# Optimization experiments

Hardware: AMD Instinct MI355X
Metric: run time of the kernel (lower is better)

The kernel has to match this reference:

```python
import jax, jax.numpy as jnp
import numpy as np

L = 8          # fixed number of instance labels (0 = background), all assumed present
DV = 0.5       # delta_v
DD = 1.5       # delta_d
LOSS_WEIGHT = 1.0


def _safe_norm(x, axis):
    sq = jnp.sum(x * x, axis=axis)
    pos = sq > 0
    return jnp.sqrt(jnp.where(pos, sq, 1.0)) * pos.astype(x.dtype)


def _per_image(emb, inst, kern, tmask):
    # emb: [D,H,W], inst: [H,W] int, kern/tmask: [H,W] float
    D, H, W = emb.shape
    HW = H * W
    tm = (tmask > 0.5).astype(inst.dtype)
    kb = (kern > 0.5).astype(inst.dtype)
    inst = inst * tm
    inst_k = (inst * kb).reshape(-1)          # kernel-region labels
    inst_f = inst.reshape(-1)                 # full-region labels
    emb_f = emb.reshape(D, -1).T              # [HW, D]

    # --- generate_coef: first/second occurrence (row-major) of each label ---
    flat = jnp.arange(HW)
    eq = inst_f[None, :] == jnp.arange(L)[:, None]          # [L, HW]
    idxs = jnp.where(eq, flat[None, :], HW)
    first = jnp.min(idxs, axis=1)
    second = jnp.min(jnp.where(idxs == first[:, None], HW, idxs), axis=1)
    first = jnp.minimum(first, HW - 1)
    second = jnp.minimum(second, HW - 1)
    r0, c0 = first // W, first % W
    r1, c1 = second // W, second % W
    # pos_id = (tmp[0,0], tmp[1,0], tmp[0,-1], tmp[1,-1]) as in the source
    pos = jnp.stack([r0, r1, c0, c1], axis=1).astype(jnp.float32)  # [L,4]
    diag = jnp.sqrt(jnp.float32(H * H + W * W))
    coef_diag = jnp.exp(jnp.sqrt((pos[:, 0] - pos[:, 2]) ** 2 +
                                 (pos[:, 1] - pos[:, 3]) ** 2) / diag / 2.0)
    zmask = (jnp.arange(L) > 0).astype(jnp.float32)          # skip label 0
    coef_diag = coef_diag * zmask
    s = pos[:, 0] + pos[:, 2]
    t = pos[:, 1] + pos[:, 3]
    dp = jnp.sqrt((s[:, None] - s[None, :]) ** 2 + (t[:, None] - t[None, :]) ** 2)
    coef_off = 1.0 - 20.0 * jnp.exp(-4.0 - 2.5 * dp / diag)
    eye = jnp.eye(L, dtype=bool)
    coef = jnp.where(eye, coef_diag[:, None], coef_off)
    coef = coef * zmask[:, None] * zmask[None, :]

    # --- per-label kernel means (segment mean) ---
    ones = jnp.ones((HW,), jnp.float32)
    cnt_k = jax.ops.segment_sum(ones, inst_k, num_segments=L)
    mean = jax.ops.segment_sum(emb_f, inst_k, num_segments=L)
    mean = mean / jnp.maximum(cnt_k, 1.0)[:, None]           # [L, D]
    mean = mean * zmask[:, None]

    # --- l_agg: per-pixel distance to own-label mean, segment-mean per label ---
    mean_px = mean[inst_f]                                   # [HW, D] gather
    dist = _safe_norm(emb_f - mean_px, axis=1)
    cd_px = coef_diag[inst_f]
    val = jnp.log(jax.nn.relu(cd_px * dist - DV) ** 2 + 1.0)
    cnt = jax.ops.segment_sum(ones, inst_f, num_segments=L)
    l_agg_per = jax.ops.segment_sum(val, inst_f, num_segments=L) / jnp.maximum(cnt, 1.0)
    l_agg = jnp.mean(l_agg_per[1:])

    # --- l_dis: coefficient-weighted pairwise hinge between means ---
    Dn = _safe_norm(mean[:, None, :] - mean[None, :, :], axis=-1)  # [L, L]
    pm = (~eye) & (zmask[:, None] > 0) & (zmask[None, :] > 0)
    vals = jnp.log(jax.nn.relu(2.0 * DD - coef * Dn) ** 2 + 1.0)
    l_dis = jnp.sum(jnp.where(pm, vals, 0.0)) / ((L - 1) * (L - 2))

    # --- l_reg ---
    l_reg = jnp.mean(jnp.log(_safe_norm(mean, axis=1) + 1.0)) * 0.001
    return l_agg + l_dis + l_reg


def reference(emb, instance, kernel, training_mask, bboxes):
    # bboxes is accepted but unused, matching the original forward_single
    loss_batch = jax.vmap(_per_image)(emb, instance, kernel, training_mask)
    return LOSS_WEIGHT * jnp.mean(loss_batch)


def setup_inputs() -> dict:
    key = jax.random.key(0)
    k1, k2, k3, k4, k5 = jax.random.split(key, 5)
    B, D, H, W = 8, 4, 640, 640
    emb = jax.random.normal(k1, (B, D, H, W), dtype=jnp.float32)
    instance = jax.random.randint(k2, (B, H, W), 0, L, dtype=jnp.int32)
    kernel = jax.random.uniform(k3, (B, H, W), dtype=jnp.float32)
    training_mask = jax.random.uniform(k4, (B, H, W), dtype=jnp.float32)
    bboxes = jax.random.uniform(k5, (B, 10, 4), dtype=jnp.float32)
    return {"emb": emb, "instance": instance, "kernel": kernel,
            "training_mask": training_mask, "bboxes": bboxes}
```

## Files before the change

### kernel.cpp

```cpp
#include <hip/hip_runtime.h>

#define B_    8
#define D_    4
#define H_    640
#define W_    640
#define HW_   (H_ * W_)
#define L_    8
#define NL    (L_ - 1)
#define BLOCK 256
#define VITER 4
#define PXB   (BLOCK * 4 * VITER)
#define GRIDX (HW_ / PXB)

__device__ __forceinline__ void gatom_add(float* p, float v) {
    unsafeAtomicAdd(p, v);
}

__device__ __forceinline__ float4 gload4f(const float* p) {
    float4 r;
    asm volatile("global_load_dwordx4 %0, %1, off" : "=v"(r) : "v"(p));
    return r;
}
__device__ __forceinline__ int4 gload4i(const int* p) {
    int4 r;
    asm volatile("global_load_dwordx4 %0, %1, off" : "=v"(r) : "v"(p));
    return r;
}
__device__ __forceinline__ uint2 gload2u(const uint2* p) {
    uint2 r;
    asm volatile("global_load_dwordx2 %0, %1, off" : "=v"(r) : "v"(p));
    return r;
}
#define WAITCNT(n) asm volatile("s_waitcnt vmcnt(" #n ")"); \
                   __builtin_amdgcn_sched_barrier(0)

__global__ void k_init(int* ib) {
    int t = threadIdx.x;
    if (t < 128) ib[t] = HW_;
    ib[128 + t] = 0;
    if (t < 137) ib[384 + t] = 0;
}

__global__ __attribute__((amdgpu_flat_work_group_size(BLOCK, BLOCK),
                          amdgpu_waves_per_eu(4, 4)))
void k_pass1(
        const float* __restrict__ emb, const int* __restrict__ inst,
        const float* __restrict__ kern, const float* __restrict__ tmask,
        int* __restrict__ firstIdx, int* __restrict__ secondIdx,
        int* __restrict__ cntf_i, int* __restrict__ cntk_i,
        float* __restrict__ sumemb, uint2* __restrict__ lblpack) {
    __shared__ int   sCnt[L_];
    __shared__ float sSum[L_ * D_];
    __shared__ int   sM1[L_], sM2[L_];

    const int tid  = threadIdx.x;
    const int lane = tid & 63;
    if (tid < L_) { sCnt[tid] = 0; sM1[tid] = HW_; sM2[tid] = HW_; }
    if (tid < L_ * D_) sSum[tid] = 0.f;
    __syncthreads();

    const int b = blockIdx.y;
    const int blockbase = blockIdx.x * PXB;
    const float* embb = emb + (size_t)b * D_ * HW_;
    const int base = b * HW_;
    const int o0 = blockbase + tid * 4;

    int4 LB[VITER]; float4 TM[VITER], KN[VITER];
    #pragma unroll
    for (int it = 0; it < VITER; ++it)
        LB[it] = gload4i(inst + base + o0 + it * (BLOCK * 4));
    #pragma unroll
    for (int it = 0; it < VITER; ++it)
        TM[it] = gload4f(tmask + base + o0 + it * (BLOCK * 4));
    #pragma unroll
    for (int it = 0; it < VITER; ++it)
        KN[it] = gload4f(kern + base + o0 + it * (BLOCK * 4));
    float4 E0[2][D_];
    #pragma unroll
    for (int s = 0; s < 2; ++s)
        #pragma unroll
        for (int d = 0; d < D_; ++d)
            E0[s][d] = gload4f(embb + d * HW_ + o0 + s * (BLOCK * 4));

    WAITCNT(8);

    int bp0 = 0, bp1 = 0, bp2 = 0, km = 0;
    unsigned int lpLo = 0, lpHi = 0;
    #pragma unroll
    for (int it = 0; it < VITER; ++it) {
        const int*   labA = (const int*)&LB[it];
        const float* tmA  = (const float*)&TM[it];
        const float* knA  = (const float*)&KN[it];
        #pragma unroll
        for (int c = 0; c < 4; ++c) {
            const int px = it * 4 + c;
            const int lf  = (tmA[c] > 0.5f) ? labA[c] : 0;
            const bool kb = (knA[c] > 0.5f);
            bp0 |= (lf & 1) << px;
            bp1 |= ((lf >> 1) & 1) << px;
            bp2 |= ((lf >> 2) & 1) << px;
            km  |= (kb ? 1 : 0) << px;
            if (px < 8) lpLo |= (unsigned int)lf << (4 * px);
            else        lpHi |= (unsigned int)lf << (4 * (px - 8));
        }
    }

    float4 E1[2][D_];
    #pragma unroll
    for (int s = 0; s < 2; ++s)
        #pragma unroll
        for (int d = 0; d < D_; ++d)
            E1[s][d] = gload4f(embb + d * HW_ + o0 + (2 + s) * (BLOCK * 4));

    WAITCNT(8);

    float sm[NL][D_];
    #pragma unroll
    for (int l = 0; l < NL; ++l)
        #pragma unroll
        for (int d = 0; d < D_; ++d) sm[l][d] = 0.f;

    #pragma unroll
    for (int s = 0; s < 2; ++s) {
        const float* e0A = (const float*)&E0[s][0];
        const float* e1A = (const float*)&E0[s][1];
        const float* e2A = (const float*)&E0[s][2];
        const float* e3A = (const float*)&E0[s][3];
        #pragma unroll
        for (int c = 0; c < 4; ++c) {
            const int px  = s * 4 + c;
            const int lf  = (int)((lpLo >> (4 * px)) & 7u);
            const int lfk = ((km >> px) & 1) ? lf : 0;
            #pragma unroll
            for (int l = 1; l < L_; ++l) {
                const float mk = (lfk == l) ? 1.0f : 0.0f;
                sm[l - 1][0] += mk * e0A[c];
                sm[l - 1][1] += mk * e1A[c];
                sm[l - 1][2] += mk * e2A[c];
                sm[l - 1][3] += mk * e3A[c];
            }
        }
    }

    WAITCNT(0);

    #pragma unroll
    for (int s = 0; s < 2; ++s) {
        const float* e0A = (const float*)&E1[s][0];
        const float* e1A = (const float*)&E1[s][1];
        const float* e2A = (const float*)&E1[s][2];
        const float* e3A = (const float*)&E1[s][3];
        #pragma unroll
        for (int c = 0; c < 4; ++c) {
            const int px  = 8 + s * 4 + c;
            const int nib = s * 4 + c;
            const int lf  = (int)((lpHi >> (4 * nib)) & 7u);
            const int lfk = ((km >> px) & 1) ? lf : 0;
            #pragma unroll
            for (int l = 1; l < L_; ++l) {
                const float mk = (lfk == l) ? 1.0f : 0.0f;
                sm[l - 1][0] += mk * e0A[c];
                sm[l - 1][1] += mk * e1A[c];
                sm[l - 1][2] += mk * e2A[c];
                sm[l - 1][3] += mk * e3A[c];
            }
        }
    }

    lblpack[(size_t)(b * GRIDX + blockIdx.x) * BLOCK + tid] = make_uint2(lpLo, lpHi);

    const int nb0 = ~bp0, nb1 = ~bp1, nb2 = ~bp2;
    int cnt[NL], m1[NL], m2[NL];
    #pragma unroll
    for (int l = 1; l < L_; ++l) {
        const int k = l - 1;
        int h = ((l & 1) ? bp0 : nb0) & ((l & 2) ? bp1 : nb1) & ((l & 4) ? bp2 : nb2);
        h &= 0xFFFF;
        cnt[k] = (__popc(h) << 16) | __popc(h & km);
        const int h2 = h & (h - 1);
        const int p1 = __ffs(h) - 1;
        const int p2 = __ffs(h2) - 1;
        m1[k] = h  ? (o0 + (p1 >> 2) * (BLOCK * 4) + (p1 & 3)) : HW_;
        m2[k] = h2 ? (o0 + (p2 >> 2) * (BLOCK * 4) + (p2 & 3)) : HW_;
    }

    #pragma unroll
    for (int l = 0; l < NL; ++l) {
        #pragma unroll
        for (int off = 32; off > 0; off >>= 1) {
            cnt[l]   += __shfl_down(cnt[l], off);
            sm[l][0] += __shfl_down(sm[l][0], off);
            sm[l][1] += __shfl_down(sm[l][1], off);
            sm[l][2] += __shfl_down(sm[l][2], off);
            sm[l][3] += __shfl_down(sm[l][3], off);
            int o1 = __shfl_down(m1[l], off);
            int o2 = __shfl_down(m2[l], off);
            m2[l] = min(min(m2[l], o2), max(m1[l], o1));
            m1[l] = min(m1[l], o1);
        }
    }
    if (lane == 0) {
        #pragma unroll
        for (int l = 0; l < NL; ++l) {
            atomicAdd(&sCnt[l + 1], cnt[l]);
            #pragma unroll
            for (int d = 0; d < D_; ++d) atomicAdd(&sSum[(l + 1) * D_ + d], sm[l][d]);
            int old = atomicMin(&sM1[l + 1], m1[l]);
            atomicMin(&sM2[l + 1], max(old, m1[l]));
            atomicMin(&sM2[l + 1], m2[l]);
        }
    }
    __syncthreads();

    if (tid >= 1 && tid < L_) {
        const int pc = sCnt[tid];
        atomicAdd(&cntf_i[b * L_ + tid], pc >> 16);
        atomicAdd(&cntk_i[b * L_ + tid], pc & 0xFFFF);
        int old = atomicMin(&firstIdx[b * L_ + tid], sM1[tid]);
        atomicMin(&secondIdx[b * L_ + tid], max(old, sM1[tid]));
        atomicMin(&secondIdx[b * L_ + tid], sM2[tid]);
    }
    if (tid >= D_ && tid < L_ * D_)
        gatom_add(&sumemb[b * L_ * D_ + tid], sSum[tid]);
}

__global__ __attribute__((amdgpu_flat_work_group_size(BLOCK, BLOCK),
                          amdgpu_waves_per_eu(4, 4)))
void k_pass3(
        const float* __restrict__ emb, const uint2* __restrict__ lblpack,
        const int* __restrict__ firstIdx, const int* __restrict__ secondIdx,
        const int* __restrict__ cntk_i, const int* __restrict__ cntf_i,
        const float* __restrict__ sumemb, float* __restrict__ sumvalb) {
    __shared__ float4 sMean[L_];
    __shared__ float  sCd[L_], sInv[L_];
    __shared__ float  sAcc;

    const int tid = threadIdx.x;
    const int b   = blockIdx.y;

    if (tid < L_) {
        float4 mu = {0.f, 0.f, 0.f, 0.f};
        float cd = 0.f, inv = 0.f;
        if (tid > 0) {
            const float invk = 1.0f / fmaxf((float)cntk_i[b * L_ + tid], 1.0f);
            mu.x = sumemb[b * L_ * D_ + tid * D_ + 0] * invk;
            mu.y = sumemb[b * L_ * D_ + tid * D_ + 1] * invk;
            mu.z = sumemb[b * L_ * D_ + tid * D_ + 2] * invk;
            mu.w = sumemb[b * L_ * D_ + tid * D_ + 3] * invk;
            const float diag = sqrtf((float)(H_ * H_ + W_ * W_));
            int f = min(firstIdx[b * L_ + tid],  HW_ - 1);
            int s = min(secondIdx[b * L_ + tid], HW_ - 1);
            float r0 = (float)(f / W_), c0 = (float)(f % W_);
            float r1 = (float)(s / W_), c1 = (float)(s % W_);
            cd = __expf(sqrtf((r0 - c0) * (r0 - c0) + (r1 - c1) * (r1 - c1))
                        / diag * 0.5f);
            inv = 1.0f / fmaxf((float)cntf_i[b * L_ + tid], 1.0f);
        }
        sMean[tid] = mu; sCd[tid] = cd; sInv[tid] = inv;
        if (tid == 0) sAcc = 0.f;
    }
    __syncthreads();

    const int blockbase = blockIdx.x * PXB;
    const float* embb = emb + (size_t)b * D_ * HW_;
    const int o0 = blockbase + tid * 4;

    const uint2 lp = gload2u(lblpack + (size_t)(b * GRIDX + blockIdx.x) * BLOCK + tid);
    float4 E[VITER][D_];
    #pragma unroll
    for (int it = 0; it < VITER; ++it)
        #pragma unroll
        for (int d = 0; d < D_; ++d)
            E[it][d] = gload4f(embb + d * HW_ + o0 + it * (BLOCK * 4));

    float acc = 0.f;
    #pragma unroll
    for (int it = 0; it < VITER; ++it) {
        if (it == 0) { WAITCNT(12); }
        else if (it == 1) { WAITCNT(8); }
        else if (it == 2) { WAITCNT(4); }
        else { WAITCNT(0); }

        const float* e0A = (const float*)&E[it][0];
        const float* e1A = (const float*)&E[it][1];
        const float* e2A = (const float*)&E[it][2];
        const float* e3A = (const float*)&E[it][3];
        #pragma unroll
        for (int c = 0; c < 4; ++c) {
            const int px = it * 4 + c;
            const int lf = (int)(((px < 8) ? (lp.x >> (4 * px))
                                           : (lp.y >> (4 * (px - 8)))) & 7u);
            const float4 mu = sMean[lf];
            float dx = e0A[c] - mu.x, dy = e1A[c] - mu.y;
            float dz = e2A[c] - mu.z, dw = e3A[c] - mu.w;
            float d2 = dx * dx + dy * dy + dz * dz + dw * dw;
            float x  = fmaxf(sCd[lf] * sqrtf(d2) - 0.5f, 0.0f);
            acc += __logf(x * x + 1.0f) * sInv[lf];
        }
    }

    #pragma unroll
    for (int off = 32; off > 0; off >>= 1)
        acc += __shfl_down(acc, off);
    if ((tid & 63) == 0) atomicAdd(&sAcc, acc);
    __syncthreads();
    if (tid == 0) gatom_add(&sumvalb[b], sAcc);
}

__global__ __launch_bounds__(512) void k_final(
        const int* __restrict__ firstIdx, const int* __restrict__ secondIdx,
        const int* __restrict__ cntk_i, const float* __restrict__ sumemb,
        const float* __restrict__ sumvalb, float* __restrict__ out) {
    __shared__ float sWave[8];
    const int tid = threadIdx.x;
    const int b = tid >> 6, ij = tid & 63, i = ij >> 3, j = ij & 7;
    const float diag = sqrtf((float)(H_ * H_ + W_ * W_));

    float mi[D_], mj[D_];
    {
        float ci = 1.0f / fmaxf((float)cntk_i[b * L_ + i], 1.0f);
        float cj = 1.0f / fmaxf((float)cntk_i[b * L_ + j], 1.0f);
        #pragma unroll
        for (int d = 0; d < D_; ++d) {
            mi[d] = (i > 0) ? sumemb[(b * L_ + i) * D_ + d] * ci : 0.0f;
            mj[d] = (j > 0) ? sumemb[(b * L_ + j) * D_ + d] * cj : 0.0f;
        }
    }

    float contrib = 0.0f;
    if (j == 0) {
        float d2 = 0.f;
        #pragma unroll
        for (int d = 0; d < D_; ++d) d2 += mi[d] * mi[d];
        float n = (d2 > 0.f) ? sqrtf(d2) : 0.f;
        contrib += __logf(n + 1.0f) * (0.001f / (float)L_);
    }
    if (i == 0 && j == 1)
        contrib += sumvalb[b] * (1.0f / (float)NL);
    if (i >= 1 && j >= 1 && i != j) {
        float d2 = 0.f;
        #pragma unroll
        for (int d = 0; d < D_; ++d) {
            float df = mi[d] - mj[d];
            d2 += df * df;
        }
        float Dn = (d2 > 0.f) ? sqrtf(d2) : 0.f;
        int fi = min(firstIdx[b * L_ + i],  HW_ - 1);
        int si = min(secondIdx[b * L_ + i], HW_ - 1);
        int fj = min(firstIdx[b * L_ + j],  HW_ - 1);
        int sj = min(secondIdx[b * L_ + j], HW_ - 1);
        float ssi = (float)(fi / W_) + (float)(fi % W_);
        float tti = (float)(si / W_) + (float)(si % W_);
        float ssj = (float)(fj / W_) + (float)(fj % W_);
        float ttj = (float)(sj / W_) + (float)(sj % W_);
        float dx = ssi - ssj, dy = tti - ttj;
        float dp = sqrtf(dx * dx + dy * dy);
        float coef = 1.0f - 20.0f * __expf(-4.0f - 2.5f * dp / diag);
        float x = fmaxf(3.0f - coef * Dn, 0.0f);
        contrib += __logf(x * x + 1.0f) * (1.0f / 42.0f);
    }

    #pragma unroll
    for (int off = 32; off > 0; off >>= 1)
        contrib += __shfl_down(contrib, off);
    if ((tid & 63) == 0) sWave[tid >> 6] = contrib;
    __syncthreads();
    if (tid == 0) {
        float t = 0.f;
        #pragma unroll
        for (int w = 0; w < 8; ++w) t += sWave[w];
        out[0] = t * (1.0f / (float)B_);
    }
}

extern "C" void kernel_launch(void* const* d_in, const int* in_sizes, int n_in,
                              void* d_out, int out_size, void* d_ws, size_t ws_size,
                              hipStream_t stream) {
    const float* emb   = (const float*)d_in[0];
    const int*   inst  = (const int*)  d_in[1];
    const float* kern  = (const float*)d_in[2];
    const float* tmask = (const float*)d_in[3];

    int*   ib        = (int*)d_ws;
    int*   firstIdx  = ib;
    int*   secondIdx = ib + 64;
    int*   cntf_i    = ib + 128;
    int*   cntk_i    = ib + 192;
    float* sumemb    = (float*)(ib + 256);
    float* sumvalb   = (float*)(ib + 512);
    uint2* lblpack   = (uint2*)(ib + 1024);
    float* out       = (float*)d_out;

    dim3 grid(GRIDX, B_);

    k_init <<<1, 256, 0, stream>>>(ib);
    k_pass1<<<grid, BLOCK, 0, stream>>>(emb, inst, kern, tmask,
                                        firstIdx, secondIdx, cntf_i, cntk_i,
                                        sumemb, lblpack);
    k_pass3<<<grid, BLOCK, 0, stream>>>(emb, lblpack, firstIdx, secondIdx,
                                        cntk_i, cntf_i, sumemb, sumvalb);
    k_final<<<1, 512, 0, stream>>>(firstIdx, secondIdx, cntk_i,
                                   sumemb, sumvalb, out);
}
```

Measured before the change: 149.2 us.

## Fuse statistics and aggregation passes with a per-image grid barrier

Merges the statistics pass and the aggregation-loss pass into one kernel. The 100 blocks of each image meet at a software barrier built from an atomic counter and a flag, then read the per-label sums with acquire atomic loads. The packed labels stay in registers instead of going to a workspace buffer and being loaded back, and one kernel launch goes away. In exchange, blocks spin-wait at the barrier, and correctness depends on all 800 blocks being resident at the same time.

```diff
diff --git a/kernel.cpp b/kernel.cpp
--- a/kernel.cpp
+++ b/kernel.cpp
@@ -15,7 +15,12 @@
 __device__ __forceinline__ void gatom_add(float* p, float v) {
     unsafeAtomicAdd(p, v);
 }
-
+__device__ __forceinline__ int aload_i(const int* p) {
+    return __hip_atomic_load(p, __ATOMIC_ACQUIRE, __HIP_MEMORY_SCOPE_AGENT);
+}
+__device__ __forceinline__ float aload_f(const float* p) {
+    return __hip_atomic_load(p, __ATOMIC_ACQUIRE, __HIP_MEMORY_SCOPE_AGENT);
+}
 __device__ __forceinline__ float4 gload4f(const float* p) {
     float4 r;
     asm volatile("global_load_dwordx4 %0, %1, off" : "=v"(r) : "v"(p));
@@ -26,11 +31,6 @@
     asm volatile("global_load_dwordx4 %0, %1, off" : "=v"(r) : "v"(p));
     return r;
 }
-__device__ __forceinline__ uint2 gload2u(const uint2* p) {
-    uint2 r;
-    asm volatile("global_load_dwordx2 %0, %1, off" : "=v"(r) : "v"(p));
-    return r;
-}
 #define WAITCNT(n) asm volatile("s_waitcnt vmcnt(" #n ")"); \
                    __builtin_amdgcn_sched_barrier(0)
 
@@ -38,20 +38,24 @@
     int t = threadIdx.x;
     if (t < 128) ib[t] = HW_;
     ib[128 + t] = 0;
-    if (t < 137) ib[384 + t] = 0;
+    if (t < 176) ib[384 + t] = 0;
 }
 
 __global__ __attribute__((amdgpu_flat_work_group_size(BLOCK, BLOCK),
                           amdgpu_waves_per_eu(4, 4)))
-void k_pass1(
+void k_fused(
         const float* __restrict__ emb, const int* __restrict__ inst,
         const float* __restrict__ kern, const float* __restrict__ tmask,
         int* __restrict__ firstIdx, int* __restrict__ secondIdx,
         int* __restrict__ cntf_i, int* __restrict__ cntk_i,
-        float* __restrict__ sumemb, uint2* __restrict__ lblpack) {
-    __shared__ int   sCnt[L_];
-    __shared__ float sSum[L_ * D_];
-    __shared__ int   sM1[L_], sM2[L_];
+        float* __restrict__ sumemb, float* __restrict__ sumvalb,
+        int* __restrict__ barCnt, int* __restrict__ barFlag) {
+    __shared__ int    sCnt[L_];
+    __shared__ float  sSum[L_ * D_];
+    __shared__ int    sM1[L_], sM2[L_];
+    __shared__ float4 sMean[L_];
+    __shared__ float  sCd[L_], sInv[L_];
+    __shared__ float  sAcc;
 
     const int tid  = threadIdx.x;
     const int lane = tid & 63;
@@ -167,8 +171,6 @@
         }
     }
 
-    lblpack[(size_t)(b * GRIDX + blockIdx.x) * BLOCK + tid] = make_uint2(lpLo, lpHi);
-
     const int nb0 = ~bp0, nb1 = ~bp1, nb2 = ~bp2;
     int cnt[NL], m1[NL], m2[NL];
     #pragma unroll
@@ -222,50 +224,46 @@
     }
     if (tid >= D_ && tid < L_ * D_)
         gatom_add(&sumemb[b * L_ * D_ + tid], sSum[tid]);
-}
-
-__global__ __attribute__((amdgpu_flat_work_group_size(BLOCK, BLOCK),
-                          amdgpu_waves_per_eu(4, 4)))
-void k_pass3(
-        const float* __restrict__ emb, const uint2* __restrict__ lblpack,
-        const int* __restrict__ firstIdx, const int* __restrict__ secondIdx,
-        const int* __restrict__ cntk_i, const int* __restrict__ cntf_i,
-        const float* __restrict__ sumemb, float* __restrict__ sumvalb) {
-    __shared__ float4 sMean[L_];
-    __shared__ float  sCd[L_], sInv[L_];
-    __shared__ float  sAcc;
-
-    const int tid = threadIdx.x;
-    const int b   = blockIdx.y;
+
+    __syncthreads();
+    if (tid == 0) {
+        __threadfence();
+        int prev = __hip_atomic_fetch_add(&barCnt[b], 1, __ATOMIC_ACQ_REL,
+                                          __HIP_MEMORY_SCOPE_AGENT);
+        if (prev == GRIDX - 1) {
+            __hip_atomic_store(&barFlag[b], 1, __ATOMIC_RELEASE,
+                               __HIP_MEMORY_SCOPE_AGENT);
+        } else {
+            while (__hip_atomic_load(&barFlag[b], __ATOMIC_ACQUIRE,
+                                     __HIP_MEMORY_SCOPE_AGENT) == 0)
+                __builtin_amdgcn_s_sleep(2);
+        }
+    }
+    __syncthreads();
 
     if (tid < L_) {
         float4 mu = {0.f, 0.f, 0.f, 0.f};
         float cd = 0.f, inv = 0.f;
         if (tid > 0) {
-            const float invk = 1.0f / fmaxf((float)cntk_i[b * L_ + tid], 1.0f);
-            mu.x = sumemb[b * L_ * D_ + tid * D_ + 0] * invk;
-            mu.y = sumemb[b * L_ * D_ + tid * D_ + 1] * invk;
-            mu.z = sumemb[b * L_ * D_ + tid * D_ + 2] * invk;
-            mu.w = sumemb[b * L_ * D_ + tid * D_ + 3] * invk;
+            const float invk = 1.0f / fmaxf((float)aload_i(&cntk_i[b * L_ + tid]), 1.0f);
+            mu.x = aload_f(&sumemb[b * L_ * D_ + tid * D_ + 0]) * invk;
+            mu.y = aload_f(&sumemb[b * L_ * D_ + tid * D_ + 1]) * invk;
+            mu.z = aload_f(&sumemb[b * L_ * D_ + tid * D_ + 2]) * invk;
+            mu.w = aload_f(&sumemb[b * L_ * D_ + tid * D_ + 3]) * invk;
             const float diag = sqrtf((float)(H_ * H_ + W_ * W_));
-            int f = min(firstIdx[b * L_ + tid],  HW_ - 1);
-            int s = min(secondIdx[b * L_ + tid], HW_ - 1);
+            int f = min(aload_i(&firstIdx[b * L_ + tid]),  HW_ - 1);
+            int s = min(aload_i(&secondIdx[b * L_ + tid]), HW_ - 1);
             float r0 = (float)(f / W_), c0 = (float)(f % W_);
             float r1 = (float)(s / W_), c1 = (float)(s % W_);
             cd = __expf(sqrtf((r0 - c0) * (r0 - c0) + (r1 - c1) * (r1 - c1))
                         / diag * 0.5f);
-            inv = 1.0f / fmaxf((float)cntf_i[b * L_ + tid], 1.0f);
+            inv = 1.0f / fmaxf((float)aload_i(&cntf_i[b * L_ + tid]), 1.0f);
         }
         sMean[tid] = mu; sCd[tid] = cd; sInv[tid] = inv;
         if (tid == 0) sAcc = 0.f;
     }
     __syncthreads();
 
-    const int blockbase = blockIdx.x * PXB;
-    const float* embb = emb + (size_t)b * D_ * HW_;
-    const int o0 = blockbase + tid * 4;
-
-    const uint2 lp = gload2u(lblpack + (size_t)(b * GRIDX + blockIdx.x) * BLOCK + tid);
     float4 E[VITER][D_];
     #pragma unroll
     for (int it = 0; it < VITER; ++it)
@@ -288,8 +286,8 @@
         #pragma unroll
         for (int c = 0; c < 4; ++c) {
             const int px = it * 4 + c;
-            const int lf = (int)(((px < 8) ? (lp.x >> (4 * px))
-                                           : (lp.y >> (4 * (px - 8)))) & 7u);
+            const int lf = (int)(((px < 8) ? (lpLo >> (4 * px))
+                                           : (lpHi >> (4 * (px - 8)))) & 7u);
             const float4 mu = sMean[lf];
             float dx = e0A[c] - mu.x, dy = e1A[c] - mu.y;
             float dz = e2A[c] - mu.z, dw = e3A[c] - mu.w;
@@ -388,17 +386,16 @@
     int*   cntk_i    = ib + 192;
     float* sumemb    = (float*)(ib + 256);
     float* sumvalb   = (float*)(ib + 512);
-    uint2* lblpack   = (uint2*)(ib + 1024);
+    int*   barCnt    = ib + 544;
+    int*   barFlag   = ib + 552;
     float* out       = (float*)d_out;
 
     dim3 grid(GRIDX, B_);
 
     k_init <<<1, 256, 0, stream>>>(ib);
-    k_pass1<<<grid, BLOCK, 0, stream>>>(emb, inst, kern, tmask,
+    k_fused<<<grid, BLOCK, 0, stream>>>(emb, inst, kern, tmask,
                                         firstIdx, secondIdx, cntf_i, cntk_i,
-                                        sumemb, lblpack);
-    k_pass3<<<grid, BLOCK, 0, stream>>>(emb, lblpack, firstIdx, secondIdx,
-                                        cntk_i, cntf_i, sumemb, sumvalb);
+                                        sumemb, sumvalb, barCnt, barFlag);
     k_final<<<1, 512, 0, stream>>>(firstIdx, secondIdx, cntk_i,
                                    sumemb, sumvalb, out);
 }
```

Result: slower. 271.8 us (+82.1%).
